# Optimization experiments

Hardware: AMD Instinct MI355X
Metric: run time of the kernel (lower is better)

Reference implementation:

```python
import jax, jax.numpy as jnp
import numpy as np

N, T, E, E2 = 10000, 32, 320000, 160000
D, H = 128, 128
SLOPE = 0.01  # LeakyReLU negative slope (args.relu)


def _lstm_dir(x, mask, Wih, Whh, b, reverse):
    # x: [N,T,D], mask: [N,T] int; returns final hidden [N,H] honoring per-seq lengths
    xs = jnp.swapaxes(x, 0, 1)                                 # [T,N,D]
    ms = jnp.swapaxes(mask, 0, 1)[..., None].astype(x.dtype)   # [T,N,1]
    Hh = Whh.shape[1]
    h0 = jnp.zeros((x.shape[0], Hh), x.dtype)

    def step(carry, tm):
        h, c = carry
        xt, mt = tm
        g = xt @ Wih.T + h @ Whh.T + b                         # [N,4H], torch gate order i,f,g,o
        i, f, gg, o = jnp.split(g, 4, axis=-1)
        i, f, o = jax.nn.sigmoid(i), jax.nn.sigmoid(f), jax.nn.sigmoid(o)
        c_new = f * c + i * jnp.tanh(gg)
        h_new = o * jnp.tanh(c_new)
        h = mt * h_new + (1.0 - mt) * h
        c = mt * c_new + (1.0 - mt) * c
        return (h, c), None

    (h, _), _ = jax.lax.scan(step, (h0, h0), (xs, ms), reverse=reverse)
    return h


def _sage(h, src, dst, Wself, Wneigh, b):
    # DGL SAGEConv, mean aggregator: h@W_self + mean_neigh(h)@W_neigh + b
    n = h.shape[0]
    msum = jax.ops.segment_sum(h[src], dst, num_segments=n)
    deg = jax.ops.segment_sum(jnp.ones((src.shape[0],), h.dtype), dst, num_segments=n)
    neigh = msum / jnp.maximum(deg, 1.0)[:, None]
    return h @ Wself + neigh @ Wneigh + b


def setup_inputs():
    key = jax.random.key(0)
    ks = jax.random.split(key, 40)
    f = lambda i, shape: jax.random.normal(ks[i], shape, jnp.float32) * 0.05
    return dict(
        inputs_s=jax.random.randint(ks[0], (N, T), 0, 128, jnp.int32),
        inputs_sm=jnp.ones((N, T), jnp.int32),
        inputs_c=jax.random.randint(ks[1], (N,), 0, 101, jnp.int32),
        inputs_co=jax.random.randint(ks[2], (N,), 0, 92, jnp.int32),
        inputs_sl=jax.random.randint(ks[3], (N,), 0, 6, jnp.int32),
        inputs_ip=jax.random.normal(ks[4], (N, 32), jnp.float32),
        blk_src=jax.random.randint(ks[5], (E,), 0, N, jnp.int32),
        blk_dst=jax.random.randint(ks[6], (E,), 0, N, jnp.int32),
        e_src=jax.random.randint(ks[7], (E2,), 0, N, jnp.int32),
        e_dst=jax.random.randint(ks[8], (E2,), 0, N, jnp.int32),
        emb_url=f(9, (128, D)), emb_cat=f(10, (101, D)), emb_cou=f(11, (92, D)), emb_sl_t=f(12, (6, D)),
        Wih_f=f(13, (4 * D, D)), Whh_f=f(14, (4 * D, D)), b_f=f(15, (4 * D,)),
        Wih_b=f(16, (4 * D, D)), Whh_b=f(17, (4 * D, D)), b_b=f(18, (4 * D,)),
        fc_lstm_W=f(19, (2 * D, D)), fc_lstm_b=f(20, (D,)),
        attnlin_W=f(21, (H, H)), attn_W=f(22, (H, 1)), attn_b=f(23, (1,)),
        W0_self=f(24, (4, D, H)), W0_neigh=f(25, (4, D, H)), b0=f(26, (4, H)),
        Wip_self=f(27, (32, H)), Wip_neigh=f(28, (32, H)), bip=f(29, (H,)),
        W1_self=f(30, (5, H, H)), W1_neigh=f(31, (5, H, H)), b1=f(32, (5, H)),
        fc_W=f(33, (2 * H, H)), fc_b=f(34, (H,)),
        fco_W=f(35, (H, 2)), fco_b=f(36, (2,)),
    )


def reference(inputs_s, inputs_sm, inputs_c, inputs_co, inputs_sl, inputs_ip,
              blk_src, blk_dst, e_src, e_dst,
              emb_url, emb_cat, emb_cou, emb_sl_t,
              Wih_f, Whh_f, b_f, Wih_b, Whh_b, b_b,
              fc_lstm_W, fc_lstm_b, attnlin_W, attn_W, attn_b,
              W0_self, W0_neigh, b0, Wip_self, Wip_neigh, bip,
              W1_self, W1_neigh, b1, fc_W, fc_b, fco_W, fco_b):
    lrelu = lambda x: jax.nn.leaky_relu(x, SLOPE)
    # --- URL encoder: embed -> bi-LSTM -> fc (dropout is identity in eval) ---
    xu = emb_url[inputs_s]                                      # [N,T,D]
    hf = _lstm_dir(xu, inputs_sm, Wih_f, Whh_f, b_f, False)     # fwd final hidden
    hb = _lstm_dir(xu, inputs_sm, Wih_b, Whh_b, b_b, True)      # bwd final hidden
    vec_url = lrelu(jnp.concatenate([hf, hb], 1) @ fc_lstm_W + fc_lstm_b)
    # --- six-stream (here five: no rules) SAGE stacks over shared blocks ---
    h4 = jnp.stack([vec_url, emb_cat[inputs_c], emb_cou[inputs_co], emb_sl_t[inputs_sl]])  # [4,N,D]
    sage_v = jax.vmap(_sage, in_axes=(0, None, None, 0, 0, 0))
    h4 = lrelu(sage_v(h4, blk_src, blk_dst, W0_self, W0_neigh, b0))
    hip = lrelu(_sage(inputs_ip, blk_src, blk_dst, Wip_self, Wip_neigh, bip))
    hs = jnp.concatenate([h4, hip[None]], 0)                    # [5,N,H]
    hs = lrelu(sage_v(hs, blk_src, blk_dst, W1_self, W1_neigh, b1))
    hs = jnp.transpose(hs, (1, 0, 2))                           # [N,5,H]
    # --- attention fusion across streams ---
    z = jnp.einsum('nsh,ho->nso', hs, attnlin_W)                # attn_linear(h_stack)
    a = jax.nn.softmax(jnp.einsum('nso,om->nsm', z, attn_W) + attn_b, axis=1)  # [N,5,1]
    h = jnp.sum(z * a, axis=1)                                  # [N,H]
    # --- per-edge gather-concat-MLP scoring (apply_edges) ---
    cat = jnp.concatenate([h[e_src], h[e_dst]], 1)              # [E2,2H]
    score = lrelu(cat @ fc_W + fc_b) @ fco_W + fco_b            # [E2,2]
    a_src = a[e_src][..., 0]                                    # [E2,5]
    attn_e = jnp.stack([a_src, a_src], axis=1)                  # [E2,2,5]
    return score, attn_e
```

## Files before the change

### kernel.cpp

```cpp
#include <hip/hip_runtime.h>
#include <hip/hip_bf16.h>
#include <stdint.h>

typedef unsigned short u16;
typedef unsigned int   u32;
typedef unsigned long long u64;
typedef __attribute__((ext_vector_type(8))) short short8;
typedef __attribute__((ext_vector_type(4))) float f32x4;
typedef __attribute__((ext_vector_type(2))) u32   u32x2;
typedef __attribute__((ext_vector_type(4))) u32   u32x4;

#define DEV static __device__ __forceinline__

constexpr int N_  = 10000;
constexpr int T_  = 32;
constexpr int E_  = 320000;
constexpr int E2_ = 160000;

DEV u16 f2bf(float f) {
    union { float f; u32 u; } v; v.f = f;
    u32 u = v.u;
    return (u16)((u + 0x7fffu + ((u >> 16) & 1u)) >> 16);
}
DEV float bf2f(u16 h) {
    union { u32 u; float f; } v; v.u = ((u32)h) << 16; return v.f;
}
DEV float asf(u32 u) {
    union { u32 u; float f; } v; v.u = u; return v.f;
}
DEV u32 cvt_pk_bf16(float lo, float hi) {
    u32 r;
    asm("v_cvt_pk_bf16_f32 %0, %1, %2" : "=v"(r) : "v"(lo), "v"(hi));
    return r;
}
DEV float lrelu(float x) { return x > 0.f ? x : 0.01f * x; }

DEV float fexp2(float x) {
#if __has_builtin(__builtin_amdgcn_exp2f)
    return __builtin_amdgcn_exp2f(x);
#else
    return exp2f(x);
#endif
}
DEV float frcp(float x) {
#if __has_builtin(__builtin_amdgcn_rcpf)
    return __builtin_amdgcn_rcpf(x);
#else
    return 1.0f / x;
#endif
}
DEV float fsig(float x)  { return frcp(1.f + fexp2(-1.4426950408889634f * x)); }
DEV float ftanh_(float x){ return 1.f - 2.f * frcp(1.f + fexp2(2.8853900817779268f * x)); }

__global__ void k_xtab(const float* __restrict__ emb,
                       const float* __restrict__ WihF, const float* __restrict__ bF,
                       const float* __restrict__ WihB, const float* __restrict__ bB,
                       u16* __restrict__ xtab) {
    int sym = blockIdx.x, dir = blockIdx.y, o = threadIdx.x;
    const float* W = dir ? WihB : WihF;
    const float* b = dir ? bB : bF;
    __shared__ float er[128];
    if (o < 128) er[o] = emb[sym * 128 + o];
    __syncthreads();
    float s = b[o];
    const float4* Wr = (const float4*)(W + (size_t)o * 128);
    for (int k4 = 0; k4 < 32; k4++) {
        float4 wv = Wr[k4];
        s += er[4*k4]   * wv.x + er[4*k4+1] * wv.y
           + er[4*k4+2] * wv.z + er[4*k4+3] * wv.w;
    }
    xtab[((size_t)(dir * 128 + sym)) * 512 + o] = f2bf(s);
}

struct WtSeg { const float* W; u16* out; int Kd, Ks, Nw, tot; };
struct WtArgs {
    WtSeg seg[9];
    int* deg; float* bias5; const float* b0; const float* bip;
};
__global__ void k_wt_all(WtArgs a) {
    if (blockIdx.y == 9) {
        int gid = blockIdx.x * 256 + threadIdx.x;
        if (gid < N_) a.deg[gid] = 0;
        int b = gid - 10240;
        if (b >= 0 && b < 640) a.bias5[b] = (b < 512) ? a.b0[b] : a.bip[b - 512];
        return;
    }
    WtSeg sg = a.seg[blockIdx.y];
    int i = blockIdx.x * 256 + threadIdx.x;
    if (i >= sg.tot) return;
    int k = i % sg.Kd, n = (i / sg.Kd) % sg.Nw, s = i / (sg.Kd * sg.Nw);
    float v = (k < sg.Ks) ? sg.W[((size_t)s * sg.Ks + k) * sg.Nw + n] : 0.f;
    sg.out[i] = f2bf(v);
}

__global__ __launch_bounds__(512, 2) void k_lstm(
    const u16* __restrict__ xtab,
    const int* __restrict__ syms,
    const int* __restrict__ smask,
    const float* __restrict__ WhhF,
    const float* __restrict__ WhhB,
    u16* __restrict__ hcat)
{
    __shared__ u16 h_buf0[2048];
    __shared__ u16 h_buf1[2048];
    __shared__ int sym_l[512];
    __shared__ int msk_l[512];
    __shared__ int anymask;

    int tid = threadIdx.x;
    int w = tid >> 6, l = tid & 63, l15 = l & 15, lg = l >> 4;
    int dir = blockIdx.y;
    int n0 = blockIdx.x * 16;
    const float* Whh = dir ? WhhB : WhhF;

    if (tid == 0) anymask = 0;
    int m0 = 0;
    for (int i = tid; i < 512; i += 512) {
        int seq = i >> 5, t = i & 31;
        int mv = smask[(size_t)n0 * 32 + i];
        sym_l[t * 16 + seq] = syms[(size_t)n0 * 32 + i];
        msk_l[t * 16 + seq] = mv;
        m0 |= (mv == 0);
    }
    for (int i = tid; i < 2048; i += 512) h_buf0[i] = 0;
    if (__ballot(m0) != 0ull && l == 0) anymask = 1;

    short8 aw[4][4];
#pragma unroll
    for (int gg = 0; gg < 4; gg++)
#pragma unroll
    for (int kk = 0; kk < 4; kk++) {
        const float* p = Whh + (size_t)(128 * gg + 16 * w + l15) * 128 + 32 * kk + 8 * lg;
        const float4* pp = (const float4*)p;
        float4 x0 = pp[0], x1 = pp[1];
        short8 v;
        v[0] = (short)f2bf(x0.x); v[1] = (short)f2bf(x0.y);
        v[2] = (short)f2bf(x0.z); v[3] = (short)f2bf(x0.w);
        v[4] = (short)f2bf(x1.x); v[5] = (short)f2bf(x1.y);
        v[6] = (short)f2bf(x1.z); v[7] = (short)f2bf(x1.w);
        aw[gg][kk] = v;
    }

    float hreg[4] = {0, 0, 0, 0};
    float creg[4] = {0, 0, 0, 0};
    int jb = 16 * w + 4 * lg;
    int wsk = 2 * w + (lg >> 1);
    int wof = (wsk * 16 + l15) * 8 + 4 * (lg & 1);
    const u16* xbase = xtab + (size_t)dir * 128 * 512 + jb;
    __syncthreads();
    bool masked = anymask != 0;

    u32x2 xt[4];
    {
        int t0 = dir ? 31 : 0;
        int sym0 = sym_l[t0 * 16 + l15];
        const u16* xr = xbase + (size_t)sym0 * 512;
#pragma unroll
        for (int gg = 0; gg < 4; gg++) xt[gg] = *(const u32x2*)(xr + gg * 128);
    }

    auto step = [&](int st, const u16* rb, u16* wb, bool wr, bool usemask) {
        int t = dir ? (31 - st) : st;

        short8 bh[4];
#pragma unroll
        for (int kk = 0; kk < 4; kk++)
            bh[kk] = *(const short8*)&rb[((kk * 4 + lg) * 16 + l15) * 8];

        f32x4 acc[4];
#pragma unroll
        for (int gg = 0; gg < 4; gg++) {
            f32x4 a = { asf(xt[gg][0] << 16), asf(xt[gg][0] & 0xffff0000u),
                        asf(xt[gg][1] << 16), asf(xt[gg][1] & 0xffff0000u) };
#pragma unroll
            for (int kk = 0; kk < 4; kk++)
                a = __builtin_amdgcn_mfma_f32_16x16x32_bf16(aw[gg][kk], bh[kk], a, 0, 0, 0);
            acc[gg] = a;
        }

        if (wr) {
            int stn = st + 1;
            int tn = dir ? (31 - stn) : stn;
            int symn = sym_l[tn * 16 + l15];
            const u16* xr = xbase + (size_t)symn * 512;
#pragma unroll
            for (int gg = 0; gg < 4; gg++) xt[gg] = *(const u32x2*)(xr + gg * 128);
        }

        if (usemask) {
            int mt_i = msk_l[t * 16 + l15];
            bool mb = mt_i != 0;
#pragma unroll
            for (int r = 0; r < 4; r++) {
                float i_ = fsig(acc[0][r]), f_ = fsig(acc[1][r]);
                float g_ = ftanh_(acc[2][r]), o_ = fsig(acc[3][r]);
                float cn = f_ * creg[r] + i_ * g_;
                float hn = o_ * ftanh_(cn);
                hreg[r] = mb ? hn : hreg[r];
                creg[r] = mb ? cn : creg[r];
            }
        } else {
#pragma unroll
            for (int r = 0; r < 4; r++) {
                float i_ = fsig(acc[0][r]), f_ = fsig(acc[1][r]);
                float g_ = ftanh_(acc[2][r]), o_ = fsig(acc[3][r]);
                float cn = f_ * creg[r] + i_ * g_;
                hreg[r] = o_ * ftanh_(cn);
                creg[r] = cn;
            }
        }
        if (wr) {
            u32x2 pk;
            pk[0] = cvt_pk_bf16(hreg[0], hreg[1]);
            pk[1] = cvt_pk_bf16(hreg[2], hreg[3]);
            *(u32x2*)&wb[wof] = pk;
            asm volatile("s_waitcnt lgkmcnt(0)" ::: "memory");
            __builtin_amdgcn_s_barrier();
        }
    };

    if (masked) {
        for (int st2 = 0; st2 < 15; st2++) {
            step(2 * st2,     h_buf0, h_buf1, true, true);
            step(2 * st2 + 1, h_buf1, h_buf0, true, true);
        }
        step(30, h_buf0, h_buf1, true, true);
        step(31, h_buf1, h_buf0, false, true);
    } else {
        for (int st2 = 0; st2 < 15; st2++) {
            step(2 * st2,     h_buf0, h_buf1, true, false);
            step(2 * st2 + 1, h_buf1, h_buf0, true, false);
        }
        step(30, h_buf0, h_buf1, true, false);
        step(31, h_buf1, h_buf0, false, false);
    }

    {
        u32x2 pk;
        pk[0] = cvt_pk_bf16(hreg[0], hreg[1]);
        pk[1] = cvt_pk_bf16(hreg[2], hreg[3]);
        *(u32x2*)&hcat[(size_t)(n0 + l15) * 256 + dir * 128 + jb] = pk;
    }
}

template<int ACT, int DUAL>
__global__ __launch_bounds__(256) void k_gemm(
    const u16* __restrict__ A1, int lda1, int soA1,
    const u16* __restrict__ A2, int lda2, int soA2,
    const u16* __restrict__ B1, int soB1,
    const u16* __restrict__ B2, int soB2,
    const float* __restrict__ bias, int soBias,
    u16* __restrict__ C, int ldc, int soC, int M, int K)
{
    int s = blockIdx.y;
    A1 += (size_t)s * soA1;
    if (DUAL) A2 += (size_t)s * soA2;
    B1 += (size_t)s * soB1;
    if (DUAL) B2 += (size_t)s * soB2;
    if (bias) bias += (size_t)s * soBias;
    C += (size_t)s * soC;

    int tid = threadIdx.x;
    int w = tid >> 6, l = tid & 63, l15 = l & 15, lg = l >> 4;
    int mbase = blockIdx.x * 64 + w * 16;
    int arow = mbase + l15; if (arow >= M) arow = M - 1;

    f32x4 acc[8];
#pragma unroll
    for (int nt = 0; nt < 8; nt++) {
        float bv = bias ? bias[16 * nt + l15] : 0.f;
        acc[nt] = (f32x4){bv, bv, bv, bv};
    }
    for (int k0 = 0; k0 < K; k0 += 32) {
        int k = k0 + 8 * lg;
        short8 a1 = *(const short8*)&A1[(size_t)arow * lda1 + k];
        short8 a2;
        if (DUAL) a2 = *(const short8*)&A2[(size_t)arow * lda2 + k];
#pragma unroll
        for (int nt = 0; nt < 8; nt++) {
            short8 b1 = *(const short8*)&B1[(size_t)(16 * nt + l15) * K + k];
            acc[nt] = __builtin_amdgcn_mfma_f32_16x16x32_bf16(a1, b1, acc[nt], 0, 0, 0);
            if (DUAL) {
                short8 b2 = *(const short8*)&B2[(size_t)(16 * nt + l15) * K + k];
                acc[nt] = __builtin_amdgcn_mfma_f32_16x16x32_bf16(a2, b2, acc[nt], 0, 0, 0);
            }
        }
    }
#pragma unroll
    for (int nt = 0; nt < 8; nt++)
#pragma unroll
    for (int r = 0; r < 4; r++) {
        int m = mbase + 4 * lg + r;
        if (m < M) {
            float v = acc[nt][r];
            if (ACT == 1) v = lrelu(v);
            C[(size_t)m * ldc + 16 * nt + l15] = f2bf(v);
        }
    }
}

__global__ __launch_bounds__(256) void k_fcpack(
    const u16* __restrict__ hcat, const u16* __restrict__ Bt,
    const float* __restrict__ bias, u16* __restrict__ F0,
    const int* __restrict__ ic, const int* __restrict__ ico,
    const int* __restrict__ isl, const float* __restrict__ ip,
    const float* __restrict__ ecat, const float* __restrict__ ecou,
    const float* __restrict__ esl, int M)
{
    if (blockIdx.y == 1) {
        int gid = blockIdx.x * 256 + threadIdx.x;
        const int TOT = N_ * 416;
        for (int i = gid; i < TOT; i += 40192) {
            int n = i / 416, c = i - n * 416;
            float v;
            if (c < 128)      v = ecat[(size_t)ic[n]  * 128 + c];
            else if (c < 256) v = ecou[(size_t)ico[n] * 128 + (c - 128)];
            else if (c < 384) v = esl [(size_t)isl[n] * 128 + (c - 256)];
            else              v = ip  [(size_t)n * 32 + (c - 384)];
            F0[(size_t)n * 544 + 128 + c] = f2bf(v);
        }
        return;
    }
    int tid = threadIdx.x;
    int w = tid >> 6, l = tid & 63, l15 = l & 15, lg = l >> 4;
    int mbase = blockIdx.x * 64 + w * 16;
    int arow = mbase + l15; if (arow >= M) arow = M - 1;

    f32x4 acc[8];
#pragma unroll
    for (int nt = 0; nt < 8; nt++) {
        float bv = bias[16 * nt + l15];
        acc[nt] = (f32x4){bv, bv, bv, bv};
    }
    for (int k0 = 0; k0 < 256; k0 += 32) {
        int k = k0 + 8 * lg;
        short8 a1 = *(const short8*)&hcat[(size_t)arow * 256 + k];
#pragma unroll
        for (int nt = 0; nt < 8; nt++) {
            short8 b1 = *(const short8*)&Bt[(size_t)(16 * nt + l15) * 256 + k];
            acc[nt] = __builtin_amdgcn_mfma_f32_16x16x32_bf16(a1, b1, acc[nt], 0, 0, 0);
        }
    }
#pragma unroll
    for (int nt = 0; nt < 8; nt++)
#pragma unroll
    for (int r = 0; r < 4; r++) {
        int m = mbase + 4 * lg + r;
        if (m < M)
            F0[(size_t)m * 544 + 16 * nt + l15] = f2bf(lrelu(acc[nt][r]));
    }
}

__global__ void k_hist(const int* __restrict__ dst, int E, int* __restrict__ deg) {
    int e = blockIdx.x * 256 + threadIdx.x;
    if (e < E) atomicAdd(&deg[dst[e]], 1);
}
__global__ void k_scan(const int* __restrict__ deg, int* __restrict__ rowptr,
                       int* __restrict__ cursor, int n) {
    __shared__ int part[1024];
    int tid = threadIdx.x;
    const int CH = 10;
    int base = tid * CH;
    int s = 0;
#pragma unroll
    for (int i = 0; i < CH; i++) { int idx = base + i; if (idx < n) s += deg[idx]; }
    part[tid] = s; __syncthreads();
    for (int off = 1; off < 1024; off <<= 1) {
        int v = (tid >= off) ? part[tid - off] : 0;
        __syncthreads();
        part[tid] += v;
        __syncthreads();
    }
    int run = part[tid] - s;
    for (int i = 0; i < CH; i++) {
        int idx = base + i;
        if (idx < n) { rowptr[idx] = run; cursor[idx] = run; run += deg[idx]; }
    }
    if (tid == 1023) rowptr[n] = part[1023];
}
__global__ void k_fill(const int* __restrict__ src, const int* __restrict__ dst, int E,
                       int* __restrict__ cursor, int* __restrict__ colsrc) {
    int e = blockIdx.x * 256 + threadIdx.x;
    if (e < E) {
        int pos = atomicAdd(&cursor[dst[e]], 1);
        colsrc[pos] = src[e];
    }
}

__global__ __launch_bounds__(256) void k_agg(const u16* __restrict__ F, int C,
                                             const int* __restrict__ rowptr,
                                             const int* __restrict__ colsrc,
                                             u16* __restrict__ out, int N) {
    __shared__ float red[4][640];
    int n = blockIdx.x;
    int tid = threadIdx.x;
    int w = tid >> 6, l = tid & 63;
    int chunks = C >> 3;
    int c0 = l, c1 = l + 64;
    bool has1 = c1 < chunks;
    float a0[8] = {0,0,0,0,0,0,0,0}, a1[8] = {0,0,0,0,0,0,0,0};
    int beg = rowptr[n], end = rowptr[n + 1];

    auto accum = [&](u32x4 v, float* a) {
#pragma unroll
        for (int j = 0; j < 4; j++) {
            u32 u = v[j];
            a[2*j]   += asf(u << 16);
            a[2*j+1] += asf(u & 0xffff0000u);
        }
    };

    int e = beg + w;
    for (; e + 4 < end; e += 8) {
        const u32x4* r0 = (const u32x4*)(F + (size_t)colsrc[e] * C);
        const u32x4* r1 = (const u32x4*)(F + (size_t)colsrc[e + 4] * C);
        u32x4 v0 = r0[c0], v1 = r1[c0];
        if (has1) {
            u32x4 u0 = r0[c1], u1 = r1[c1];
            accum(v0, a0); accum(v1, a0);
            accum(u0, a1); accum(u1, a1);
        } else {
            accum(v0, a0); accum(v1, a0);
        }
    }
    if (e < end) {
        const u32x4* r0 = (const u32x4*)(F + (size_t)colsrc[e] * C);
        accum(r0[c0], a0);
        if (has1) accum(r0[c1], a1);
    }

    *(float4*)&red[w][8 * c0]     = (float4){a0[0], a0[1], a0[2], a0[3]};
    *(float4*)&red[w][8 * c0 + 4] = (float4){a0[4], a0[5], a0[6], a0[7]};
    if (has1) {
        *(float4*)&red[w][8 * c1]     = (float4){a1[0], a1[1], a1[2], a1[3]};
        *(float4*)&red[w][8 * c1 + 4] = (float4){a1[4], a1[5], a1[6], a1[7]};
    }
    __syncthreads();

    int dg = end - beg; if (dg < 1) dg = 1;
    float inv = 1.f / (float)dg;
    int hc = C >> 2;
    if (tid < hc) {
        float4 s0 = *(const float4*)&red[0][4 * tid];
        float4 s1 = *(const float4*)&red[1][4 * tid];
        float4 s2 = *(const float4*)&red[2][4 * tid];
        float4 s3 = *(const float4*)&red[3][4 * tid];
        float x = (s0.x + s1.x + s2.x + s3.x) * inv;
        float y = (s0.y + s1.y + s2.y + s3.y) * inv;
        float z = (s0.z + s1.z + s2.z + s3.z) * inv;
        float wv = (s0.w + s1.w + s2.w + s3.w) * inv;
        u32x2 pk; pk[0] = cvt_pk_bf16(x, y); pk[1] = cvt_pk_bf16(z, wv);
        *(u32x2*)&out[(size_t)n * C + 4 * tid] = pk;
    }
}

__global__ __launch_bounds__(320) void k_zattn(
    const u16* __restrict__ H1,
    const u16* __restrict__ Bt,
    const float* __restrict__ attnW,
    float* __restrict__ aOut,
    u16* __restrict__ hT)
{
    constexpr int ZP = 136;
    __shared__ u16 zl[80 * ZP];
    int tid = threadIdx.x;
    int w = tid >> 6, l = tid & 63, l15 = l & 15, lg = l >> 4;
    int rbase = blockIdx.x * 80 + w * 16;

    f32x4 acc[8];
#pragma unroll
    for (int nt = 0; nt < 8; nt++) acc[nt] = (f32x4){0.f, 0.f, 0.f, 0.f};
    for (int k0 = 0; k0 < 128; k0 += 32) {
        int k = k0 + 8 * lg;
        short8 a1 = *(const short8*)&H1[(size_t)(rbase + l15) * 128 + k];
#pragma unroll
        for (int nt = 0; nt < 8; nt++) {
            short8 b1 = *(const short8*)&Bt[(size_t)(16 * nt + l15) * 128 + k];
            acc[nt] = __builtin_amdgcn_mfma_f32_16x16x32_bf16(a1, b1, acc[nt], 0, 0, 0);
        }
    }
#pragma unroll
    for (int nt = 0; nt < 8; nt++)
#pragma unroll
    for (int r = 0; r < 4; r++)
        zl[(w * 16 + 4 * lg + r) * ZP + 16 * nt + l15] = f2bf(acc[nt][r]);
    __syncthreads();

    if (tid < 256) {
        int node = tid >> 4;
        int j = tid & 15;
        int d0 = j * 8;
        float4 wa0 = *(const float4*)(attnW + d0);
        float4 wa1 = *(const float4*)(attnW + d0 + 4);
        float z[5][8], lgt[5];
#pragma unroll
        for (int s = 0; s < 5; s++) {
            const u16* zr = &zl[(node * 5 + s) * ZP + d0];
            u32x4 v = *(const u32x4*)zr;
#pragma unroll
            for (int q = 0; q < 4; q++) {
                z[s][2*q]   = asf(v[q] << 16);
                z[s][2*q+1] = asf(v[q] & 0xffff0000u);
            }
            float p = z[s][0]*wa0.x + z[s][1]*wa0.y + z[s][2]*wa0.z + z[s][3]*wa0.w
                    + z[s][4]*wa1.x + z[s][5]*wa1.y + z[s][6]*wa1.z + z[s][7]*wa1.w;
#pragma unroll
            for (int m = 1; m < 16; m <<= 1) p += __shfl_xor(p, m, 64);
            lgt[s] = p;
        }
        float mx = lgt[0];
#pragma unroll
        for (int s = 1; s < 5; s++) mx = fmaxf(mx, lgt[s]);
        float ex[5], sum = 0.f;
#pragma unroll
        for (int s = 0; s < 5; s++) { ex[s] = __expf(lgt[s] - mx); sum += ex[s]; }
        float inv = 1.f / sum;
        float a[5];
#pragma unroll
        for (int s = 0; s < 5; s++) a[s] = ex[s] * inv;
        float h[8] = {0,0,0,0,0,0,0,0};
#pragma unroll
        for (int s = 0; s < 5; s++)
#pragma unroll
            for (int q = 0; q < 8; q++) h[q] += a[s] * z[s][q];
        int gn = blockIdx.x * 16 + node;
        u32x4 o;
#pragma unroll
        for (int q = 0; q < 4; q++) o[q] = cvt_pk_bf16(h[2*q], h[2*q+1]);
        *(u32x4*)&hT[(size_t)gn * 128 + d0] = o;
        if (j == 0) {
#pragma unroll
            for (int s = 0; s < 5; s++) aOut[(size_t)gn * 5 + s] = a[s];
        }
    }
}

__global__ __launch_bounds__(256) void k_edge(const u16* __restrict__ hT,
                                              const int* __restrict__ esrc,
                                              const int* __restrict__ edst,
                                              const u16* __restrict__ fcWt,
                                              const float* __restrict__ fcb,
                                              const float* __restrict__ fcoW,
                                              const float* __restrict__ fcob,
                                              const float* __restrict__ aA,
                                              float* __restrict__ score,
                                              float* __restrict__ attne,
                                              int E2) {
    int tid = threadIdx.x;
    int w = tid >> 6, l = tid & 63, l15 = l & 15, lg = l >> 4;
    int eb = (blockIdx.x * 4 + w) * 16;
    int arow = eb + l15; if (arow >= E2) arow = E2 - 1;
    int sn = esrc[arow], dn = edst[arow];

    f32x4 acc[8];
#pragma unroll
    for (int nt = 0; nt < 8; nt++) {
        float bv = fcb[16 * nt + l15];
        acc[nt] = (f32x4){bv, bv, bv, bv};
    }
#pragma unroll
    for (int kk = 0; kk < 8; kk++) {
        int k = 32 * kk + 8 * lg;
        const u16* ap = (k < 128) ? &hT[(size_t)sn * 128 + k]
                                  : &hT[(size_t)dn * 128 + (k - 128)];
        short8 a = *(const short8*)ap;
#pragma unroll
        for (int nt = 0; nt < 8; nt++) {
            short8 b = *(const short8*)&fcWt[(size_t)(16 * nt + l15) * 256 + k];
            acc[nt] = __builtin_amdgcn_mfma_f32_16x16x32_bf16(a, b, acc[nt], 0, 0, 0);
        }
    }
    float p0[4] = {0,0,0,0}, p1[4] = {0,0,0,0};
#pragma unroll
    for (int nt = 0; nt < 8; nt++) {
        int c = 16 * nt + l15;
        float w0 = fcoW[c * 2], w1 = fcoW[c * 2 + 1];
#pragma unroll
        for (int r = 0; r < 4; r++) {
            float hd = lrelu(acc[nt][r]);
            p0[r] += hd * w0; p1[r] += hd * w1;
        }
    }
#pragma unroll
    for (int m = 1; m < 16; m <<= 1) {
#pragma unroll
        for (int r = 0; r < 4; r++) {
            p0[r] += __shfl_xor(p0[r], m, 64);
            p1[r] += __shfl_xor(p1[r], m, 64);
        }
    }
    if (l15 == 0) {
        float b0v = fcob[0], b1v = fcob[1];
#pragma unroll
        for (int r = 0; r < 4; r++) {
            int e = eb + 4 * lg + r;
            if (e < E2) {
                score[(size_t)e * 2 + 0] = p0[r] + b0v;
                score[(size_t)e * 2 + 1] = p1[r] + b1v;
            }
        }
    }
#pragma unroll
    for (int pass = 0; pass < 3; pass++) {
        int idx = pass * 64 + l;
        if (idx < 160) {
            int e = eb + idx / 10;
            int j = idx % 10;
            int s = esrc[e];
            attne[(size_t)e * 10 + j] = aA[(size_t)s * 5 + (j >= 5 ? j - 5 : j)];
        }
    }
}

extern "C" void kernel_launch(void* const* d_in, const int* in_sizes, int n_in,
                              void* d_out, int out_size, void* d_ws, size_t ws_size,
                              hipStream_t stream) {
    const int* inp_s   = (const int*)d_in[0];
    const int* inp_sm  = (const int*)d_in[1];
    const int* inp_c   = (const int*)d_in[2];
    const int* inp_co  = (const int*)d_in[3];
    const int* inp_sl  = (const int*)d_in[4];
    const float* inp_ip = (const float*)d_in[5];
    const int* blk_src = (const int*)d_in[6];
    const int* blk_dst = (const int*)d_in[7];
    const int* e_src   = (const int*)d_in[8];
    const int* e_dst   = (const int*)d_in[9];
    const float* emb_url = (const float*)d_in[10];
    const float* emb_cat = (const float*)d_in[11];
    const float* emb_cou = (const float*)d_in[12];
    const float* emb_sl  = (const float*)d_in[13];
    const float* Wih_f = (const float*)d_in[14];
    const float* Whh_f = (const float*)d_in[15];
    const float* b_f   = (const float*)d_in[16];
    const float* Wih_b = (const float*)d_in[17];
    const float* Whh_b = (const float*)d_in[18];
    const float* b_b   = (const float*)d_in[19];
    const float* fc_lstm_W = (const float*)d_in[20];
    const float* fc_lstm_b = (const float*)d_in[21];
    const float* attnlin_W = (const float*)d_in[22];
    const float* attn_W    = (const float*)d_in[23];
    const float* W0_self  = (const float*)d_in[25];
    const float* W0_neigh = (const float*)d_in[26];
    const float* b0       = (const float*)d_in[27];
    const float* Wip_self  = (const float*)d_in[28];
    const float* Wip_neigh = (const float*)d_in[29];
    const float* bip       = (const float*)d_in[30];
    const float* W1_self  = (const float*)d_in[31];
    const float* W1_neigh = (const float*)d_in[32];
    const float* b1       = (const float*)d_in[33];
    const float* fc_W  = (const float*)d_in[34];
    const float* fc_b  = (const float*)d_in[35];
    const float* fco_W = (const float*)d_in[36];
    const float* fco_b = (const float*)d_in[37];

    char* ws = (char*)d_ws;
    size_t off = 0;
    auto alloc = [&](size_t bytes) -> char* {
        char* p = ws + off;
        off += (bytes + 255) & ~(size_t)255;
        return p;
    };
    u16* xtab      = (u16*)alloc((size_t)2 * 128 * 512 * 2);
    u16* hcat      = (u16*)alloc((size_t)N_ * 256 * 2);
    u16* wt_fclstm = (u16*)alloc((size_t)128 * 256 * 2);
    u16* wt_w05s   = (u16*)alloc((size_t)5 * 128 * 128 * 2);
    u16* wt_w05n   = (u16*)alloc((size_t)5 * 128 * 128 * 2);
    u16* wt_w1s    = (u16*)alloc((size_t)5 * 128 * 128 * 2);
    u16* wt_w1n    = (u16*)alloc((size_t)5 * 128 * 128 * 2);
    u16* wt_attn   = (u16*)alloc((size_t)128 * 128 * 2);
    u16* wt_fc     = (u16*)alloc((size_t)128 * 256 * 2);
    float* bias5   = (float*)alloc((size_t)5 * 128 * 4);
    u16* F0        = (u16*)alloc((size_t)N_ * 544 * 2);
    u16* NEI       = (u16*)alloc((size_t)N_ * 640 * 2);
    u16* F1        = (u16*)alloc((size_t)N_ * 640 * 2);
    u16* H1        = (u16*)alloc((size_t)N_ * 640 * 2);
    u16* hT        = (u16*)alloc((size_t)N_ * 128 * 2);
    float* aA      = (float*)alloc((size_t)N_ * 5 * 4);
    int* deg       = (int*)alloc((size_t)N_ * 4);
    int* rowptr    = (int*)alloc((size_t)(N_ + 1) * 4);
    int* cursor    = (int*)alloc((size_t)N_ * 4);
    int* colsrc    = (int*)alloc((size_t)E_ * 4);
    (void)ws_size; (void)in_sizes; (void)n_in; (void)out_size;

    float* out_score = (float*)d_out;
    float* out_attne = out_score + (size_t)2 * E2_;

    k_xtab<<<dim3(128, 2), dim3(512), 0, stream>>>(emb_url, Wih_f, b_f, Wih_b, b_b, xtab);
    {
        WtArgs a;
        a.seg[0] = {fc_lstm_W, wt_fclstm,            256, 256, 128, 1 * 128 * 256};
        a.seg[1] = {W0_self,   wt_w05s,              128, 128, 128, 4 * 128 * 128};
        a.seg[2] = {W0_neigh,  wt_w05n,              128, 128, 128, 4 * 128 * 128};
        a.seg[3] = {Wip_self,  wt_w05s + 4 * 16384,  128,  32, 128, 1 * 128 * 128};
        a.seg[4] = {Wip_neigh, wt_w05n + 4 * 16384,  128,  32, 128, 1 * 128 * 128};
        a.seg[5] = {W1_self,   wt_w1s,               128, 128, 128, 5 * 128 * 128};
        a.seg[6] = {W1_neigh,  wt_w1n,               128, 128, 128, 5 * 128 * 128};
        a.seg[7] = {attnlin_W, wt_attn,              128, 128, 128, 1 * 128 * 128};
        a.seg[8] = {fc_W,      wt_fc,                256, 256, 128, 1 * 128 * 256};
        a.deg = deg; a.bias5 = bias5; a.b0 = b0; a.bip = bip;
        k_wt_all<<<dim3((5 * 128 * 128 + 255) / 256, 10), dim3(256), 0, stream>>>(a);
    }

    k_hist<<<dim3((E_ + 255) / 256), dim3(256), 0, stream>>>(blk_dst, E_, deg);
    k_scan<<<dim3(1), dim3(1024), 0, stream>>>(deg, rowptr, cursor, N_);
    k_fill<<<dim3((E_ + 255) / 256), dim3(256), 0, stream>>>(blk_src, blk_dst, E_, cursor, colsrc);

    k_lstm<<<dim3(N_ / 16, 2), dim3(512), 0, stream>>>(xtab, inp_s, inp_sm, Whh_f, Whh_b, hcat);

    k_fcpack<<<dim3((N_ + 63) / 64, 2), dim3(256), 0, stream>>>(
        hcat, wt_fclstm, fc_lstm_b, F0,
        inp_c, inp_co, inp_sl, inp_ip, emb_cat, emb_cou, emb_sl, N_);

    k_agg<<<dim3(N_), dim3(256), 0, stream>>>(F0, 544, rowptr, colsrc, NEI, N_);
    k_gemm<1, 1><<<dim3((N_ + 63) / 64, 5), dim3(256), 0, stream>>>(
        F0, 544, 128, NEI, 544, 128, wt_w05s, 128 * 128, wt_w05n, 128 * 128,
        bias5, 128, F1, 640, 128, N_, 128);

    k_agg<<<dim3(N_), dim3(256), 0, stream>>>(F1, 640, rowptr, colsrc, NEI, N_);
    k_gemm<1, 1><<<dim3((N_ + 63) / 64, 5), dim3(256), 0, stream>>>(
        F1, 640, 128, NEI, 640, 128, wt_w1s, 128 * 128, wt_w1n, 128 * 128,
        b1, 128, H1, 640, 128, N_, 128);

    k_zattn<<<dim3(N_ / 16), dim3(320), 0, stream>>>(H1, wt_attn, attn_W, aA, hT);

    k_edge<<<dim3(E2_ / 64), dim3(256), 0, stream>>>(hT, e_src, e_dst, wt_fc, fc_b,
                                                     fco_W, fco_b, aA,
                                                     out_score, out_attne, E2_);
}
```

Baseline: 576.1 us.

## Split neighbor aggregation into one wave per node per column slice

The mean-aggregation kernel used to give each node a 256-thread block, with four waves splitting the edge list and a shared-memory reduction at the end. It now gives each wave one node and one 64-word column slice, launched on a second grid dimension of 5. Each lane accumulates a packed bf16 pair over all edges, with eight independent gathers in flight, and writes the mean directly, so the shared-memory reduction and barrier go away. To fit this fixed 320-word layout, the F0 row stride is padded from 544 to 640. That adds extra gathered traffic on padding columns in the first layer, and each gather load is narrower (4 bytes instead of 16).

```diff
diff --git a/kernel.cpp b/kernel.cpp
--- a/kernel.cpp
+++ b/kernel.cpp
@@ -317,7 +317,7 @@
             else if (c < 256) v = ecou[(size_t)ico[n] * 128 + (c - 128)];
             else if (c < 384) v = esl [(size_t)isl[n] * 128 + (c - 256)];
             else              v = ip  [(size_t)n * 32 + (c - 384)];
-            F0[(size_t)n * 544 + 128 + c] = f2bf(v);
+            F0[(size_t)n * 640 + 128 + c] = f2bf(v);
         }
         return;
     }
@@ -347,7 +347,7 @@
     for (int r = 0; r < 4; r++) {
         int m = mbase + 4 * lg + r;
         if (m < M)
-            F0[(size_t)m * 544 + 16 * nt + l15] = f2bf(lrelu(acc[nt][r]));
+            F0[(size_t)m * 640 + 16 * nt + l15] = f2bf(lrelu(acc[nt][r]));
     }
 }
 
@@ -387,71 +387,41 @@
     }
 }
 
-__global__ __launch_bounds__(256) void k_agg(const u16* __restrict__ F, int C,
+__global__ __launch_bounds__(256) void k_agg(const u16* __restrict__ F,
                                              const int* __restrict__ rowptr,
                                              const int* __restrict__ colsrc,
                                              u16* __restrict__ out, int N) {
-    __shared__ float red[4][640];
-    int n = blockIdx.x;
-    int tid = threadIdx.x;
-    int w = tid >> 6, l = tid & 63;
-    int chunks = C >> 3;
-    int c0 = l, c1 = l + 64;
-    bool has1 = c1 < chunks;
-    float a0[8] = {0,0,0,0,0,0,0,0}, a1[8] = {0,0,0,0,0,0,0,0};
+    int w = threadIdx.x >> 6, l = threadIdx.x & 63;
+    int n = blockIdx.x * 4 + w;
+    if (n >= N) return;
+    int cu = blockIdx.y * 64 + l;
+    const u32* Fc = (const u32*)F;
     int beg = rowptr[n], end = rowptr[n + 1];
-
-    auto accum = [&](u32x4 v, float* a) {
-#pragma unroll
-        for (int j = 0; j < 4; j++) {
-            u32 u = v[j];
-            a[2*j]   += asf(u << 16);
-            a[2*j+1] += asf(u & 0xffff0000u);
-        }
-    };
-
-    int e = beg + w;
-    for (; e + 4 < end; e += 8) {
-        const u32x4* r0 = (const u32x4*)(F + (size_t)colsrc[e] * C);
-        const u32x4* r1 = (const u32x4*)(F + (size_t)colsrc[e + 4] * C);
-        u32x4 v0 = r0[c0], v1 = r1[c0];
-        if (has1) {
-            u32x4 u0 = r0[c1], u1 = r1[c1];
-            accum(v0, a0); accum(v1, a0);
-            accum(u0, a1); accum(u1, a1);
-        } else {
-            accum(v0, a0); accum(v1, a0);
-        }
-    }
-    if (e < end) {
-        const u32x4* r0 = (const u32x4*)(F + (size_t)colsrc[e] * C);
-        accum(r0[c0], a0);
-        if (has1) accum(r0[c1], a1);
-    }
-
-    *(float4*)&red[w][8 * c0]     = (float4){a0[0], a0[1], a0[2], a0[3]};
-    *(float4*)&red[w][8 * c0 + 4] = (float4){a0[4], a0[5], a0[6], a0[7]};
-    if (has1) {
-        *(float4*)&red[w][8 * c1]     = (float4){a1[0], a1[1], a1[2], a1[3]};
-        *(float4*)&red[w][8 * c1 + 4] = (float4){a1[4], a1[5], a1[6], a1[7]};
-    }
-    __syncthreads();
+    float a0 = 0.f, a1 = 0.f;
+
+    int e = beg;
+    for (; e + 8 <= end; e += 8) {
+        int s[8];
+#pragma unroll
+        for (int j = 0; j < 8; j++) s[j] = colsrc[e + j];
+        u32 v[8];
+#pragma unroll
+        for (int j = 0; j < 8; j++) v[j] = Fc[(size_t)s[j] * 320 + cu];
+#pragma unroll
+        for (int j = 0; j < 8; j++) {
+            a0 += asf(v[j] << 16);
+            a1 += asf(v[j] & 0xffff0000u);
+        }
+    }
+    for (; e < end; e++) {
+        u32 v = Fc[(size_t)colsrc[e] * 320 + cu];
+        a0 += asf(v << 16);
+        a1 += asf(v & 0xffff0000u);
+    }
 
     int dg = end - beg; if (dg < 1) dg = 1;
     float inv = 1.f / (float)dg;
-    int hc = C >> 2;
-    if (tid < hc) {
-        float4 s0 = *(const float4*)&red[0][4 * tid];
-        float4 s1 = *(const float4*)&red[1][4 * tid];
-        float4 s2 = *(const float4*)&red[2][4 * tid];
-        float4 s3 = *(const float4*)&red[3][4 * tid];
-        float x = (s0.x + s1.x + s2.x + s3.x) * inv;
-        float y = (s0.y + s1.y + s2.y + s3.y) * inv;
-        float z = (s0.z + s1.z + s2.z + s3.z) * inv;
-        float wv = (s0.w + s1.w + s2.w + s3.w) * inv;
-        u32x2 pk; pk[0] = cvt_pk_bf16(x, y); pk[1] = cvt_pk_bf16(z, wv);
-        *(u32x2*)&out[(size_t)n * C + 4 * tid] = pk;
-    }
+    ((u32*)out)[(size_t)n * 320 + cu] = cvt_pk_bf16(a0 * inv, a1 * inv);
 }
 
 __global__ __launch_bounds__(320) void k_zattn(
@@ -670,7 +640,7 @@
     u16* wt_attn   = (u16*)alloc((size_t)128 * 128 * 2);
     u16* wt_fc     = (u16*)alloc((size_t)128 * 256 * 2);
     float* bias5   = (float*)alloc((size_t)5 * 128 * 4);
-    u16* F0        = (u16*)alloc((size_t)N_ * 544 * 2);
+    u16* F0        = (u16*)alloc((size_t)N_ * 640 * 2);
     u16* NEI       = (u16*)alloc((size_t)N_ * 640 * 2);
     u16* F1        = (u16*)alloc((size_t)N_ * 640 * 2);
     u16* H1        = (u16*)alloc((size_t)N_ * 640 * 2);
@@ -711,12 +681,12 @@
         hcat, wt_fclstm, fc_lstm_b, F0,
         inp_c, inp_co, inp_sl, inp_ip, emb_cat, emb_cou, emb_sl, N_);
 
-    k_agg<<<dim3(N_), dim3(256), 0, stream>>>(F0, 544, rowptr, colsrc, NEI, N_);
+    k_agg<<<dim3((N_ + 3) / 4, 5), dim3(256), 0, stream>>>(F0, rowptr, colsrc, NEI, N_);
     k_gemm<1, 1><<<dim3((N_ + 63) / 64, 5), dim3(256), 0, stream>>>(
-        F0, 544, 128, NEI, 544, 128, wt_w05s, 128 * 128, wt_w05n, 128 * 128,
+        F0, 640, 128, NEI, 640, 128, wt_w05s, 128 * 128, wt_w05n, 128 * 128,
         bias5, 128, F1, 640, 128, N_, 128);
 
-    k_agg<<<dim3(N_), dim3(256), 0, stream>>>(F1, 640, rowptr, colsrc, NEI, N_);
+    k_agg<<<dim3((N_ + 3) / 4, 5), dim3(256), 0, stream>>>(F1, rowptr, colsrc, NEI, N_);
     k_gemm<1, 1><<<dim3((N_ + 63) / 64, 5), dim3(256), 0, stream>>>(
         F1, 640, 128, NEI, 640, 128, wt_w1s, 128 * 128, wt_w1n, 128 * 128,
         b1, 128, H1, 640, 128, N_, 128);
```

Result: no change. 572.4 us, median of 2 (-0.6%).
